# Kernel tuning notes

Hardware: AMD Instinct MI355X
Metric: run time of the kernel (lower is better)

Reference implementation:

```python
import jax, jax.numpy as jnp
import numpy as np

V, E, H, L, K, T = 100000, 512, 256, 2, 48, 2048
START, END = 46, 47
NEG = -10000.0


def _lstm_dir(x, wih, whh, bih, bhh):
    # x: (T, In); wih: (4H, In); whh: (4H, H) -> hs: (T, H). Gate order i,f,g,o (PyTorch).
    h0 = jnp.zeros((H,), x.dtype)
    c0 = jnp.zeros((H,), x.dtype)
    xg = x @ wih.T + (bih + bhh)  # precompute input gates: (T, 4H)
    def step(carry, xt):
        h, c = carry
        g = xt + h @ whh.T
        i, f, gg, o = jnp.split(g, 4)
        c = jax.nn.sigmoid(f) * c + jax.nn.sigmoid(i) * jnp.tanh(gg)
        h = jax.nn.sigmoid(o) * jnp.tanh(c)
        return (h, c), h
    _, hs = jax.lax.scan(step, (h0, c0), xg)
    return hs


def _bilstm_feats(sentence, embedding, w_ih, w_hh, b_ih, b_hh, W_out, b_out):
    x = embedding[sentence]  # (T, E)
    for l in range(w_ih.shape[0]):
        hf = _lstm_dir(x, w_ih[l, 0], w_hh[l, 0], b_ih[l, 0], b_hh[l, 0])
        hb = _lstm_dir(x[::-1], w_ih[l, 1], w_hh[l, 1], b_ih[l, 1], b_hh[l, 1])[::-1]
        x = jnp.concatenate([hf, hb], axis=-1)  # (T, 2H)
    return x @ W_out.T + b_out  # (T, K)


def _viterbi(feats, transitions):
    init = jnp.full((K,), NEG, feats.dtype).at[START].set(0.0)
    def step(fv, feat):
        scores = fv[None, :] + transitions  # (K_next, K_prev)
        best_prev = jnp.argmax(scores, axis=1)
        fv = jnp.max(scores, axis=1) + feat
        return fv, best_prev
    fv, bptrs = jax.lax.scan(step, init, feats)  # bptrs: (T, K)
    terminal = fv + transitions[END]
    best_last = jnp.argmax(terminal)
    path_score = terminal[best_last]
    def back(carry, bp):
        return bp[carry], carry
    _, rev_path = jax.lax.scan(back, best_last, bptrs[::-1])
    return path_score, rev_path[::-1]  # tags for t = 0..T-1


def setup_inputs() -> dict:
    key = jax.random.key(0)
    ks = jax.random.split(key, 9)
    s = 0.05
    transitions = jax.random.normal(ks[7], (K, K), jnp.float32)
    transitions = transitions.at[START, :].set(NEG).at[:, END].set(NEG)
    return {
        "sentence": jax.random.randint(ks[0], (T,), 0, V),
        "embedding": jax.random.normal(ks[1], (V, E), jnp.float32) * s,
        "w_ih": jax.random.normal(ks[2], (L, 2, 4 * H, E), jnp.float32) * s,
        "w_hh": jax.random.normal(ks[3], (L, 2, 4 * H, H), jnp.float32) * s,
        "b_ih": jax.random.normal(ks[4], (L, 2, 4 * H), jnp.float32) * s,
        "b_hh": jax.random.normal(ks[5], (L, 2, 4 * H), jnp.float32) * s,
        "W_out": jax.random.normal(ks[6], (K, 2 * H), jnp.float32) * s,
        "b_out": jnp.zeros((K,), jnp.float32),
        "transitions": transitions,
    }


def reference(sentence, embedding, w_ih, w_hh, b_ih, b_hh, W_out, b_out, transitions):
    feats = _bilstm_feats(sentence, embedding, w_ih, w_hh, b_ih, b_hh, W_out, b_out)
    score, path = _viterbi(feats, transitions)
    return score, path
```

## Files before the change

### kernel.cpp

```cpp
#include <hip/hip_runtime.h>
#include <hip/hip_bf16.h>

#define T_LEN 2048
#define E_DIM 512
#define H_DIM 256
#define K_TAG 48
#define START_TAG 46
#define END_TAG 47
#define NEG_VAL -10000.0f

__global__ __launch_bounds__(256) void gemm_xg(
    const float* __restrict__ Abase, const int* __restrict__ sent,
    const float* __restrict__ Bw, const float* __restrict__ bih,
    const float* __restrict__ bhh, float* __restrict__ out, int useGather)
{
    __shared__ float As[16][68];
    __shared__ float Bs[16][68];
    const int tx = threadIdx.x & 15, ty = threadIdx.x >> 4;
    const int t0 = blockIdx.y * 64, n0 = blockIdx.x * 64;
    const int r  = threadIdx.x >> 2;
    const int kq = (threadIdx.x & 3) * 4;
    const float* arow;
    if (useGather) arow = Abase + (size_t)sent[t0 + r] * 512 + kq;
    else           arow = Abase + (size_t)(t0 + r) * 512 + kq;
    const float* brow = Bw + (size_t)(n0 + r) * 512 + kq;

    float acc[4][4];
#pragma unroll
    for (int i = 0; i < 4; i++)
#pragma unroll
        for (int j = 0; j < 4; j++) acc[i][j] = 0.f;

    for (int k0 = 0; k0 < 512; k0 += 16) {
        float4 a4 = *(const float4*)(arow + k0);
        float4 b4 = *(const float4*)(brow + k0);
        __syncthreads();
        As[kq+0][r] = a4.x; As[kq+1][r] = a4.y; As[kq+2][r] = a4.z; As[kq+3][r] = a4.w;
        Bs[kq+0][r] = b4.x; Bs[kq+1][r] = b4.y; Bs[kq+2][r] = b4.z; Bs[kq+3][r] = b4.w;
        __syncthreads();
#pragma unroll
        for (int k = 0; k < 16; k++) {
            float4 av = *(const float4*)&As[k][ty*4];
            float4 bv = *(const float4*)&Bs[k][tx*4];
            acc[0][0] = fmaf(av.x, bv.x, acc[0][0]); acc[0][1] = fmaf(av.x, bv.y, acc[0][1]);
            acc[0][2] = fmaf(av.x, bv.z, acc[0][2]); acc[0][3] = fmaf(av.x, bv.w, acc[0][3]);
            acc[1][0] = fmaf(av.y, bv.x, acc[1][0]); acc[1][1] = fmaf(av.y, bv.y, acc[1][1]);
            acc[1][2] = fmaf(av.y, bv.z, acc[1][2]); acc[1][3] = fmaf(av.y, bv.w, acc[1][3]);
            acc[2][0] = fmaf(av.z, bv.x, acc[2][0]); acc[2][1] = fmaf(av.z, bv.y, acc[2][1]);
            acc[2][2] = fmaf(av.z, bv.z, acc[2][2]); acc[2][3] = fmaf(av.z, bv.w, acc[2][3]);
            acc[3][0] = fmaf(av.w, bv.x, acc[3][0]); acc[3][1] = fmaf(av.w, bv.y, acc[3][1]);
            acc[3][2] = fmaf(av.w, bv.z, acc[3][2]); acc[3][3] = fmaf(av.w, bv.w, acc[3][3]);
        }
    }
#pragma unroll
    for (int i = 0; i < 4; i++) {
        int t = t0 + ty*4 + i;
#pragma unroll
        for (int j = 0; j < 4; j++) {
            int n = n0 + tx*4 + j;
            float b = bih[n] + bhh[n];
            out[((size_t)((n >> 10) * 2048 + t) << 10) + (n & 1023)] = acc[i][j] + b;
        }
    }
}

__global__ __launch_bounds__(512)
__attribute__((amdgpu_waves_per_eu(2, 2)))
void lstm_pass(
    const float* __restrict__ xg,
    const float* __restrict__ whh,
    float* __restrict__ xout,
    unsigned long long* __restrict__ pairs)
{
    const int tid = threadIdx.x;
    const int w = tid >> 6, L = tid & 63;
    const int d = blockIdx.x >> 2, b = blockIdx.x & 3;
    const int g = w >> 1, c = w & 1;

    __shared__ __align__(16) float stage[2][256];
    __shared__ float parts[8][64];

    float wr[128];
    {
        const float* wp = whh + ((size_t)d << 18) +
                          (size_t)(g * 256 + b * 64 + L) * 256 + c * 128;
#pragma unroll
        for (int i = 0; i < 32; i++) {
            float4 v = ((const float4*)wp)[i];
            wr[4*i+0] = v.x; wr[4*i+1] = v.y; wr[4*i+2] = v.z; wr[4*i+3] = v.w;
        }
    }
#pragma unroll
    for (int i = 0; i < 128; i++)
        asm volatile("" : "+v"(wr[i]));

    unsigned long long* mypairs = pairs + (size_t)d * 512;
    const float* xgd = xg + ((size_t)d << 21);

    float cst = 0.f;
    float xgp[4] = {0.f, 0.f, 0.f, 0.f};
    if (w == 7) {
        stage[1][b*64 + L] = 0.f;
        int t0 = (d == 0) ? 0 : (T_LEN - 1);
#pragma unroll
        for (int g2 = 0; g2 < 4; g2++)
            xgp[g2] = xgd[((size_t)t0 << 10) + g2*256 + b*64 + L];
    }
    const int pc = (w < 3) ? (w + (w >= b)) : 0;

    for (int s = 1; s <= T_LEN; s++) {
        const int par = s & 1;
        if (w < 3) {
            unsigned long long* pp = mypairs + ((s-1) & 1) * 256 + pc*64 + L;
            const unsigned tagexp = (unsigned)(s - 1);
            unsigned long long v;
            for (;;) {
                v = __hip_atomic_load(pp, __ATOMIC_RELAXED, __HIP_MEMORY_SCOPE_AGENT);
                if (__all((unsigned)(v >> 32) == tagexp)) break;
            }
            stage[par][pc*64 + L] = __uint_as_float((unsigned)v);
        }
        __syncthreads();

        const float4* hv = (const float4*)&stage[par][c*128];
        float acc[4] = {0.f, 0.f, 0.f, 0.f};
#pragma unroll
        for (int k4 = 0; k4 < 32; k4++) {
            float4 h4 = hv[k4];
            acc[k4 & 3] = fmaf(h4.x, wr[4*k4+0], acc[k4 & 3]);
            acc[k4 & 3] = fmaf(h4.y, wr[4*k4+1], acc[k4 & 3]);
            acc[k4 & 3] = fmaf(h4.z, wr[4*k4+2], acc[k4 & 3]);
            acc[k4 & 3] = fmaf(h4.w, wr[4*k4+3], acc[k4 & 3]);
        }
        parts[w][L] = (acc[0] + acc[1]) + (acc[2] + acc[3]);
        __syncthreads();

        if (w == 7) {
            float G[4];
#pragma unroll
            for (int g2 = 0; g2 < 4; g2++)
                G[g2] = parts[2*g2][L] + parts[2*g2+1][L] + xgp[g2];
            float ig = 1.f / (1.f + __expf(-G[0]));
            float fg = 1.f / (1.f + __expf(-G[1]));
            float e2 = __expf(2.f * G[2]);
            float tg = (e2 - 1.f) / (e2 + 1.f);
            float og = 1.f / (1.f + __expf(-G[3]));
            cst = fg * cst + ig * tg;
            float ec = __expf(2.f * cst);
            float th = (ec - 1.f) / (ec + 1.f);
            float h = og * th;
            __hip_atomic_store(mypairs + par*256 + b*64 + L,
                ((unsigned long long)(unsigned)s << 32) | (unsigned long long)__float_as_uint(h),
                __ATOMIC_RELAXED, __HIP_MEMORY_SCOPE_AGENT);
            stage[1 - par][b*64 + L] = h;
            int t = (d == 0) ? (s - 1) : (T_LEN - s);
            xout[(size_t)t * 512 + d*256 + b*64 + L] = h;
            int tn = (d == 0) ? ((s < T_LEN) ? s : (T_LEN - 1))
                              : ((s < T_LEN) ? (T_LEN - 1 - s) : 0);
#pragma unroll
            for (int g2 = 0; g2 < 4; g2++)
                xgp[g2] = xgd[((size_t)tn << 10) + g2*256 + b*64 + L];
        }
    }
}

__global__ __launch_bounds__(64) void feats_kern(
    const float* __restrict__ x2, const float* __restrict__ Wout,
    const float* __restrict__ bout, float* __restrict__ feats)
{
    const int t = blockIdx.x;
    __shared__ __align__(16) float xr[512];
    for (int i = threadIdx.x; i < 128; i += 64)
        ((float4*)xr)[i] = ((const float4*)(x2 + (size_t)t * 512))[i];
    __syncthreads();
    const int n = threadIdx.x;
    if (n < K_TAG) {
        const float4* wrow = (const float4*)(Wout + (size_t)n * 512);
        float acc = 0.f;
#pragma unroll 8
        for (int k4 = 0; k4 < 128; k4++) {
            float4 wv = wrow[k4];
            float4 xv = ((const float4*)xr)[k4];
            acc = fmaf(wv.x, xv.x, acc); acc = fmaf(wv.y, xv.y, acc);
            acc = fmaf(wv.z, xv.z, acc); acc = fmaf(wv.w, xv.w, acc);
        }
        feats[t * K_TAG + n] = acc + bout[n];
    }
}

__global__ __launch_bounds__(64) void viterbi_kern(
    const float* __restrict__ feats, const float* __restrict__ trans,
    unsigned char* __restrict__ bptr, int* __restrict__ bnd,
    float* __restrict__ out)
{
    const int lane = threadIdx.x;
    const bool act = lane < K_TAG;
    float tr[K_TAG];
#pragma unroll
    for (int p = 0; p < K_TAG; p++)
        tr[p] = act ? trans[lane * K_TAG + p] : -3.0e38f;

    float fv = (lane == START_TAG) ? 0.f : NEG_VAL;
    int orig = lane;
    float feat = act ? feats[lane] : 0.f;

    for (int t = 0; t < T_LEN; t++) {
        float featn = (act && (t + 1 < T_LEN)) ? feats[(t + 1) * K_TAG + lane] : 0.f;
        float m = -3.0e38f; int bp = 0;
#pragma unroll
        for (int p = 0; p < K_TAG; p++) {
            float sp = __uint_as_float(__builtin_amdgcn_readlane(__float_as_uint(fv), p));
            float sc = sp + tr[p];
            if (sc > m) { m = sc; bp = p; }
        }
        fv = m + feat;
        feat = featn;
        if (act) bptr[t * K_TAG + lane] = (unsigned char)bp;
        orig = __shfl(orig, bp);
        if ((t & 127) == 127) {
            if (act) bnd[(t >> 7) * K_TAG + lane] = orig;
            orig = lane;
        }
    }
    float term = fv + (act ? trans[END_TAG * K_TAG + lane] : -3.0e38f);
    float bm = -3.0e38f; int bl = 0;
#pragma unroll
    for (int p = 0; p < K_TAG; p++) {
        float v = __uint_as_float(__builtin_amdgcn_readlane(__float_as_uint(term), p));
        if (v > bm) { bm = v; bl = p; }
    }
    if (lane == 0) out[0] = bm;

    __shared__ int sb[16];
    if (lane == 0) {
        int s = bl;
        sb[15] = s;
        for (int k = 15; k >= 1; k--) { s = bnd[k * K_TAG + s]; sb[k - 1] = s; }
    }
    __syncthreads();
    if (lane < 16) {
        int s = sb[lane];
        for (int t = lane * 128 + 127; t >= lane * 128; t--) {
            out[1 + t] = (float)s;
            s = (int)bptr[t * K_TAG + s];
        }
    }
}

extern "C" void kernel_launch(void* const* d_in, const int* in_sizes, int n_in,
                              void* d_out, int out_size, void* d_ws, size_t ws_size,
                              hipStream_t stream) {
    const int*   sent = (const int*)d_in[0];
    const float* emb  = (const float*)d_in[1];
    const float* wih  = (const float*)d_in[2];
    const float* whh  = (const float*)d_in[3];
    const float* bih  = (const float*)d_in[4];
    const float* bhh  = (const float*)d_in[5];
    const float* Wout = (const float*)d_in[6];
    const float* bout = (const float*)d_in[7];
    const float* trans= (const float*)d_in[8];
    float* out = (float*)d_out;

    float* ws = (float*)d_ws;
    float* xg    = ws;
    float* x1    = xg + 4194304;
    float* x2    = x1 + 1048576;
    float* feats = x2 + 1048576;
    unsigned long long* pairs = (unsigned long long*)(feats + 98304);
    unsigned char* bptr = (unsigned char*)(pairs + 2048);
    int* bnd = (int*)(bptr + T_LEN * K_TAG);

    hipMemsetAsync(pairs, 0, 2048 * sizeof(unsigned long long), stream);

    dim3 gg(32, 32);
    gemm_xg<<<gg, 256, 0, stream>>>(emb, sent, wih, bih, bhh, xg, 1);
    lstm_pass<<<8, 512, 0, stream>>>(xg, whh, x1, pairs);
    gemm_xg<<<gg, 256, 0, stream>>>(x1, nullptr, wih + (1 << 20),
                                    bih + 2048, bhh + 2048, xg, 0);
    lstm_pass<<<8, 512, 0, stream>>>(xg, whh + (1 << 19), x2, pairs + 1024);
    feats_kern<<<T_LEN, 64, 0, stream>>>(x2, Wout, bout, feats);
    viterbi_kern<<<1, 64, 0, stream>>>(feats, trans, bptr, bnd, out);
}
```

Measured before the change: 10.63 ms.

## Co-locate LSTM recurrence blocks on one XCD for faster cross-block handoff

Launches 64 blocks instead of 8. Each block reads its XCC id from a hardware register, and a rendezvous picks the 8 blocks that share one XCD; the other blocks exit. On that XCD the per-step hidden-state exchange uses sc0-scoped global loads and stores, which should stay in the shared L2 instead of going through device-scope coherence, cutting the latency of each of the 2048 sequential steps. It keeps a spin budget that falls back to agent-scope atomics, and it reuses the bptr workspace for the rendezvous slots. This risks deadlock or stale reads if the co-residency assumptions fail.

```diff
diff --git a/kernel.cpp b/kernel.cpp
--- a/kernel.cpp
+++ b/kernel.cpp
@@ -70,15 +70,89 @@
     const float* __restrict__ xg,
     const float* __restrict__ whh,
     float* __restrict__ xout,
-    unsigned long long* __restrict__ pairs)
+    unsigned long long* __restrict__ pairs,
+    unsigned long long* __restrict__ rdv)
 {
     const int tid = threadIdx.x;
-    const int w = tid >> 6, L = tid & 63;
-    const int d = blockIdx.x >> 2, b = blockIdx.x & 3;
-    const int g = w >> 1, c = w & 1;
 
     __shared__ __align__(16) float stage[2][256];
     __shared__ float parts[8][64];
+    __shared__ int sh_dec[2];
+
+    {
+        unsigned xcc;
+        asm volatile("s_getreg_b32 %0, hwreg(20, 0, 32)" : "=s"(xcc));
+        xcc &= 0xfu;
+        if (tid == 0)
+            __hip_atomic_store(rdv + blockIdx.x,
+                               (1ull << 32) | (unsigned long long)xcc,
+                               __ATOMIC_RELAXED, __HIP_MEMORY_SCOPE_AGENT);
+
+        if (blockIdx.x == 0 && tid < 64) {
+            unsigned long long r = 0;
+            bool got = false;
+            for (int it = 0; it < 32768; ++it) {
+                r = __hip_atomic_load(rdv + tid, __ATOMIC_RELAXED,
+                                      __HIP_MEMORY_SCOPE_AGENT);
+                if (__all((unsigned)(r >> 32) == 1u)) { got = true; break; }
+            }
+            unsigned long long mask = 0ull;
+            if (got) {
+                const unsigned x_i = (unsigned)r & 0xfu;
+                const unsigned target =
+                    (unsigned)__builtin_amdgcn_readfirstlane((int)x_i) & 0xfu;
+                bool valid = true;
+                unsigned long long mm = 0ull;
+                for (unsigned x = 0; x < 8; x++) {
+                    unsigned long long m = __ballot(x_i == x);
+                    if (__popcll(m) != 8) valid = false;
+                    if (x == target) mm = m;
+                }
+                if (valid) mask = mm;
+            }
+            if (tid == 0) {
+                __hip_atomic_store(rdv + 64, (2ull << 32) | (mask & 0xffffffffull),
+                                   __ATOMIC_RELAXED, __HIP_MEMORY_SCOPE_AGENT);
+                __hip_atomic_store(rdv + 65, (2ull << 32) | (mask >> 32),
+                                   __ATOMIC_RELAXED, __HIP_MEMORY_SCOPE_AGENT);
+            }
+        }
+
+        if (tid == 0) {
+            unsigned long long lo, hi;
+            do {
+                lo = __hip_atomic_load(rdv + 64, __ATOMIC_RELAXED,
+                                       __HIP_MEMORY_SCOPE_AGENT);
+            } while ((unsigned)(lo >> 32) != 2u);
+            do {
+                hi = __hip_atomic_load(rdv + 65, __ATOMIC_RELAXED,
+                                       __HIP_MEMORY_SCOPE_AGENT);
+            } while ((unsigned)(hi >> 32) != 2u);
+            const unsigned long long mask =
+                (lo & 0xffffffffull) | ((hi & 0xffffffffull) << 32);
+            const int bid = (int)blockIdx.x;
+            int fs, wd;
+            if (mask != 0ull) {
+                fs = 1;
+                if ((mask >> bid) & 1ull)
+                    wd = __popcll(mask & ((1ull << bid) - 1ull));
+                else wd = -1;
+            } else {
+                fs = 0;
+                wd = (bid < 8) ? bid : -1;
+            }
+            sh_dec[0] = fs;
+            sh_dec[1] = wd;
+        }
+        __syncthreads();
+    }
+    const int fast = sh_dec[0];
+    const int wid  = sh_dec[1];
+    if (wid < 0) return;
+
+    const int w = tid >> 6, L = tid & 63;
+    const int d = wid >> 2, b = wid & 3;
+    const int g = w >> 1, c = w & 1;
 
     float wr[128];
     {
@@ -108,15 +182,31 @@
     }
     const int pc = (w < 3) ? (w + (w >= b)) : 0;
 
+    int use_fast = fast;
+    int budget   = 16384;
+
     for (int s = 1; s <= T_LEN; s++) {
         const int par = s & 1;
         if (w < 3) {
             unsigned long long* pp = mypairs + ((s-1) & 1) * 256 + pc*64 + L;
             const unsigned tagexp = (unsigned)(s - 1);
-            unsigned long long v;
-            for (;;) {
-                v = __hip_atomic_load(pp, __ATOMIC_RELAXED, __HIP_MEMORY_SCOPE_AGENT);
-                if (__all((unsigned)(v >> 32) == tagexp)) break;
+            unsigned long long v = 0;
+            if (use_fast) {
+                for (;;) {
+                    asm volatile(
+                        "global_load_dwordx2 %0, %1, off sc0\n\t"
+                        "s_waitcnt vmcnt(0)"
+                        : "=&v"(v) : "v"((unsigned long long)pp) : "memory");
+                    if (__all((unsigned)(v >> 32) == tagexp)) break;
+                    if (--budget < 0) { use_fast = 0; break; }
+                }
+            }
+            if (!use_fast) {
+                for (;;) {
+                    v = __hip_atomic_load(pp, __ATOMIC_RELAXED,
+                                          __HIP_MEMORY_SCOPE_AGENT);
+                    if (__all((unsigned)(v >> 32) == tagexp)) break;
+                }
             }
             stage[par][pc*64 + L] = __uint_as_float((unsigned)v);
         }
@@ -149,9 +239,19 @@
             float ec = __expf(2.f * cst);
             float th = (ec - 1.f) / (ec + 1.f);
             float h = og * th;
-            __hip_atomic_store(mypairs + par*256 + b*64 + L,
-                ((unsigned long long)(unsigned)s << 32) | (unsigned long long)__float_as_uint(h),
-                __ATOMIC_RELAXED, __HIP_MEMORY_SCOPE_AGENT);
+            const unsigned long long pv =
+                ((unsigned long long)(unsigned)s << 32) |
+                (unsigned long long)__float_as_uint(h);
+            unsigned long long* pa = mypairs + par*256 + b*64 + L;
+            if (fast) {
+                asm volatile("global_store_dwordx2 %0, %1, off sc0"
+                             :: "v"((unsigned long long)pa), "v"(pv) : "memory");
+                __hip_atomic_store(pa, pv, __ATOMIC_RELAXED,
+                                   __HIP_MEMORY_SCOPE_AGENT);
+            } else {
+                __hip_atomic_store(pa, pv, __ATOMIC_RELAXED,
+                                   __HIP_MEMORY_SCOPE_AGENT);
+            }
             stage[1 - par][b*64 + L] = h;
             int t = (d == 0) ? (s - 1) : (T_LEN - s);
             xout[(size_t)t * 512 + d*256 + b*64 + L] = h;
@@ -269,15 +369,16 @@
     unsigned long long* pairs = (unsigned long long*)(feats + 98304);
     unsigned char* bptr = (unsigned char*)(pairs + 2048);
     int* bnd = (int*)(bptr + T_LEN * K_TAG);
-
-    hipMemsetAsync(pairs, 0, 2048 * sizeof(unsigned long long), stream);
+    unsigned long long* rdv = (unsigned long long*)bptr;
+
+    hipMemsetAsync(pairs, 0, (2048 + 144) * sizeof(unsigned long long), stream);
 
     dim3 gg(32, 32);
     gemm_xg<<<gg, 256, 0, stream>>>(emb, sent, wih, bih, bhh, xg, 1);
-    lstm_pass<<<8, 512, 0, stream>>>(xg, whh, x1, pairs);
+    lstm_pass<<<64, 512, 0, stream>>>(xg, whh, x1, pairs, rdv);
     gemm_xg<<<gg, 256, 0, stream>>>(x1, nullptr, wih + (1 << 20),
                                     bih + 2048, bhh + 2048, xg, 0);
-    lstm_pass<<<8, 512, 0, stream>>>(xg, whh + (1 << 19), x2, pairs + 1024);
+    lstm_pass<<<64, 512, 0, stream>>>(xg, whh + (1 << 19), x2, pairs + 1024, rdv + 72);
     feats_kern<<<T_LEN, 64, 0, stream>>>(x2, Wout, bout, feats);
     viterbi_kern<<<1, 64, 0, stream>>>(feats, trans, bptr, bnd, out);
 }
```

Result: slower. 16.63 ms (+56.5%).
